# Kernel tuning notes

Measured on AMD Instinct MI355X. Metric: run time of the kernel, lower is better.

Reference implementation:

```python
import jax, jax.numpy as jnp
import numpy as np

GAMMA = 1.0          # smoothing parameter (init default)
NORMALIZE = False    # init default
BIG = 1e10           # finite stand-in for +inf boundary (exp(-BIG/gamma) == 0, grad-safe)


def setup_inputs() -> dict:
    key = jax.random.key(0)
    k1, k2 = jax.random.split(key)
    B, T, D = 64, 1024, 8
    pred = jax.random.normal(k1, (B, T, D), dtype=jnp.float32)
    target = jax.random.normal(k2, (B, T, D), dtype=jnp.float32)
    return {"pred": pred, "target": target}


def _soft_dtw(dist, gamma):
    # dist: [B, T, T] pairwise squared distances. Returns R[:, -1, -1] of shape [B].
    B, T, _ = dist.shape
    inv_g = 1.0 / gamma

    def inner_step(r_left, inp):
        # r_left = R[i, j-1]; r0 = R[i-1, j-1]; r1 = R[i-1, j]; d = D[i-1, j-1]
        r0, r1, d = inp  # each [B]
        stack = jnp.stack([r0, r1, r_left], axis=-1)          # [B, 3]
        rmin = -gamma * jax.nn.logsumexp(-stack * inv_g, axis=-1)
        val = d + rmin
        return val, val

    def outer_step(prev_row, d_row):
        # prev_row: [B, T+1] = R[i-1, :]; d_row: [B, T] = D[i-1, :]
        xs = (prev_row[:, :-1].T, prev_row[:, 1:].T, d_row.T)  # each [T, B]
        r_init = jnp.full((B,), BIG, dist.dtype)               # R[i, 0] = inf
        _, vals = jax.lax.scan(inner_step, r_init, xs)         # vals: [T, B]
        new_row = jnp.concatenate(
            [jnp.full((B, 1), BIG, dist.dtype), vals.T], axis=1)  # [B, T+1]
        return new_row, None

    # R[0, 0] = 0, R[0, j>0] = inf
    row0 = jnp.concatenate(
        [jnp.zeros((B, 1), dist.dtype), jnp.full((B, T), BIG, dist.dtype)], axis=1)
    last_row, _ = jax.lax.scan(outer_step, row0, jnp.transpose(dist, (1, 0, 2)))
    return last_row[:, -1]  # R[:, T, T]


def reference(pred, target):
    B, T, D = pred.shape
    # [B, T, T] squared Euclidean distance between all time-step pairs
    dist = jnp.sum((pred[:, :, None, :] - target[:, None, :, :]) ** 2, axis=-1)
    loss = _soft_dtw(dist, GAMMA)  # [B]
    if NORMALIZE:
        loss = loss / T
    return jnp.mean(loss)
```

## Files before the change

kernel.cpp:

```cpp
#include <hip/hip_runtime.h>


typedef float v2f __attribute__((ext_vector_type(2)));

static constexpr int T      = 1024;
static constexpr int NB     = 64;
static constexpr int NTH    = 256;
static constexpr int NW     = 4;
static constexpr int CT     = 2;
static constexpr int NQ     = T / CT;
static constexpr int WSTEPS = NQ + 63;

#define BIGF 1e10f
#define L2EF 1.4426950408889634f
#define LN2F 0.6931471805599453f

__device__ __forceinline__ float fexp2(float x) { return __builtin_amdgcn_exp2f(x); }
__device__ __forceinline__ float flog2(float x) { return __builtin_amdgcn_logf(x); }

__device__ __forceinline__ float softmin2(float a, float b, float c) {
  float m = fminf(fminf(a, b), c);
  float M = fmaxf(fmaxf(a, b), c);
  float e = __builtin_amdgcn_fmed3f(a, b, c);
  float s = fexp2(m - e) + fexp2(m - M);
  return m - flog2(1.0f + s);
}

__device__ __forceinline__ v2f pkfma(v2f a, v2f b, v2f c) {
  v2f d;
  asm("v_pk_fma_f32 %0, %1, %2, %3" : "=v"(d) : "v"(a), "v"(b), "v"(c));
  return d;
}

__device__ __forceinline__ v2f lo2(const float4& c) { v2f r; r.x = c.x; r.y = c.y; return r; }
__device__ __forceinline__ v2f hi2(const float4& c) { v2f r; r.x = c.z; r.y = c.w; return r; }

__device__ __forceinline__ v2f dotpk(v2f seed, const v2f* pp, const float4* C) {
  v2f a = seed;
  a = pkfma(pp[0], lo2(C[0]), a);
  a = pkfma(pp[1], hi2(C[0]), a);
  a = pkfma(pp[2], lo2(C[1]), a);
  a = pkfma(pp[3], hi2(C[1]), a);
  a = pkfma(pp[4], lo2(C[2]), a);
  a = pkfma(pp[5], hi2(C[2]), a);
  a = pkfma(pp[6], lo2(C[3]), a);
  a = pkfma(pp[7], hi2(C[3]), a);
  return a;
}

#define STEP(SW, CUR, NXT)                                                   \
  {                                                                          \
    const int sw_ = (SW);                                                    \
    float2 cb = make_float2(BIGF, BIGF);                                     \
    if (w > 0 && sw_ < NQ) {                                                 \
      if ((sw_ & 3) == 0) {                                                  \
        const int need = ((sw_ + 3 < NQ) ? sw_ + 3 : NQ - 1) + 63;           \
        while (seen < need) {                                                 \
          seen = __hip_atomic_load(&prog_s[w - 1], __ATOMIC_ACQUIRE,         \
                                   __HIP_MEMORY_SCOPE_WORKGROUP);            \
          if (seen < need) __builtin_amdgcn_s_sleep(1);                      \
        }                                                                    \
      }                                                                      \
      cb = buf_s[(w - 1) * NQ + sw_];       \
    }                                                                        \
    float na0 = __shfl_up(vD0, 1, 64);                                       \
    float na1 = __shfl_up(vD1, 1, 64);                                       \
    float a0 = (lane == 0) ? cb.x : na0;                                     \
    float a1 = (lane == 0) ? cb.y : na1;                                     \
    const int q = sw_ - lane;                                                \
    {            \
      int qn = sw_ + 1 - lane;                                               \
      qn = qn < 0 ? 0 : (qn > NQ - 1 ? NQ - 1 : qn);                         \
      const float4* bp = &tgt4_s[qn * 5];                                    \
      NXT[0] = bp[0]; NXT[1] = bp[1]; NXT[2] = bp[2]; NXT[3] = bp[3];        \
      NXT[4] = bp[4];                                                        \
    }                                                                        \
    if (q >= 0 && q < NQ) {                                                  \
      const float tn0 = CUR[4].x, tn1 = CUR[4].y;                            \
      v2f sA; sA.x = pnA + tn0; sA.y = pnA + tn1;                            \
      v2f sB; sB.x = pnB + tn0; sB.y = pnB + tn1;                            \
      v2f sC; sC.x = pnC + tn0; sC.y = pnC + tn1;                            \
      v2f sD; sD.x = pnD + tn0; sD.y = pnD + tn1;                            \
      v2f accA = dotpk(sA, ppA, CUR);                                        \
      v2f accB = dotpk(sB, ppB, CUR);                                        \
      v2f accC = dotpk(sC, ppC, CUR);                                        \
      v2f accD = dotpk(sD, ppD, CUR);                                        \
      float vA0 = accA.x + softmin2(carry, a0, lA);                          \
      float vA1 = accA.y + softmin2(a0, a1, vA0);                            \
      float vB0 = accB.x + softmin2(lA, vA0, lB);                            \
      float vB1 = accB.y + softmin2(vA0, vA1, vB0);                          \
      float vC0 = accC.x + softmin2(lB, vB0, lC);                            \
      float vC1 = accC.y + softmin2(vB0, vB1, vC0);                          \
      vD0 = accD.x + softmin2(lC, vC0, lD);                                  \
      vD1 = accD.y + softmin2(vC0, vC1, vD0);                                \
      lA = vA1; lB = vB1; lC = vC1; lD = vD1; carry = a1;                    \
      if (lane == 63 && w < NW - 1)                                          \
        buf_s[w * NQ + q] = make_float2(vD0, vD1);                           \
      if (t == NTH - 1 && q == NQ - 1) ws[b] = vD1 * LN2F;                   \
    }                                                                        \
    if (lane == 63 && w < NW - 1 && ((sw_ & 3) == 3 || sw_ == WSTEPS - 1))   \
      __hip_atomic_store(&prog_s[w], sw_, __ATOMIC_RELEASE,                  \
                         __HIP_MEMORY_SCOPE_WORKGROUP);                      \
  }

__global__ __launch_bounds__(NTH) void sdtw_kernel(const float* __restrict__ pred,
                                                   const float* __restrict__ target,
                                                   float* __restrict__ ws) {
  __shared__ float4 tgt4_s[NQ * 5];
  __shared__ float2 buf_s[(NW - 1) * NQ];
  __shared__ int prog_s[NW];

  const int t    = threadIdx.x;
  const int w    = t >> 6;
  const int lane = t & 63;
  const int b    = blockIdx.x;
  const float* pr = pred + (size_t)b * T * 8;
  const float* tg = target + (size_t)b * T * 8;

  {
    const float4* tg4 = reinterpret_cast<const float4*>(tg);
    const float s = -2.0f * L2EF;
#pragma unroll
    for (int h = 0; h < 2; ++h) {
      float4 u0 = tg4[t * 8 + 4 * h + 0];
      float4 u1 = tg4[t * 8 + 4 * h + 1];
      float4 u2 = tg4[t * 8 + 4 * h + 2];
      float4 u3 = tg4[t * 8 + 4 * h + 3];
      float tA = (u0.x * u0.x + u0.y * u0.y) + (u0.z * u0.z + u0.w * u0.w) +
                 (u1.x * u1.x + u1.y * u1.y) + (u1.z * u1.z + u1.w * u1.w);
      float tB = (u2.x * u2.x + u2.y * u2.y) + (u2.z * u2.z + u2.w * u2.w) +
                 (u3.x * u3.x + u3.y * u3.y) + (u3.z * u3.z + u3.w * u3.w);
      float4* dst = &tgt4_s[(2 * t + h) * 5];
      dst[0] = make_float4(u0.x * s, u2.x * s, u0.y * s, u2.y * s);
      dst[1] = make_float4(u0.z * s, u2.z * s, u0.w * s, u2.w * s);
      dst[2] = make_float4(u1.x * s, u3.x * s, u1.y * s, u3.y * s);
      dst[3] = make_float4(u1.z * s, u3.z * s, u1.w * s, u3.w * s);
      dst[4] = make_float4(tA * L2EF, tB * L2EF, 0.0f, 0.0f);
    }
  }
  if (t < NW) prog_s[t] = -1;

  const float4* pr4 = reinterpret_cast<const float4*>(pr);
  float4 qA0 = pr4[t * 8 + 0], qA1 = pr4[t * 8 + 1];
  float4 qB0 = pr4[t * 8 + 2], qB1 = pr4[t * 8 + 3];
  float4 qC0 = pr4[t * 8 + 4], qC1 = pr4[t * 8 + 5];
  float4 qD0 = pr4[t * 8 + 6], qD1 = pr4[t * 8 + 7];
#define NRM(a, b)                                                            \
  (((a.x * a.x + a.y * a.y) + (a.z * a.z + a.w * a.w) +                      \
    (b.x * b.x + b.y * b.y) + (b.z * b.z + b.w * b.w)) * L2EF)
  float pnA = NRM(qA0, qA1), pnB = NRM(qB0, qB1);
  float pnC = NRM(qC0, qC1), pnD = NRM(qD0, qD1);
#define DUP(pp, r0, r1)                                                      \
  pp[0].x = r0.x; pp[0].y = r0.x; pp[1].x = r0.y; pp[1].y = r0.y;            \
  pp[2].x = r0.z; pp[2].y = r0.z; pp[3].x = r0.w; pp[3].y = r0.w;            \
  pp[4].x = r1.x; pp[4].y = r1.x; pp[5].x = r1.y; pp[5].y = r1.y;            \
  pp[6].x = r1.z; pp[6].y = r1.z; pp[7].x = r1.w; pp[7].y = r1.w;
  v2f ppA[8], ppB[8], ppC[8], ppD[8];
  DUP(ppA, qA0, qA1) DUP(ppB, qB0, qB1) DUP(ppC, qC0, qC1) DUP(ppD, qD0, qD1)

  __syncthreads();

  float lA = BIGF, lB = BIGF, lC = BIGF, lD = BIGF;
  float carry = (t == 0) ? 0.0f : BIGF;
  float vD0 = BIGF, vD1 = BIGF;
  int seen = -1;

  float4 tgA[5], tgB[5];
  {
    tgA[0] = tgt4_s[0]; tgA[1] = tgt4_s[1]; tgA[2] = tgt4_s[2];
    tgA[3] = tgt4_s[3]; tgA[4] = tgt4_s[4];
  }

  for (int sw = 0; sw < 576; sw += 2) {
    STEP(sw, tgA, tgB)
    STEP(sw + 1, tgB, tgA)
  }
}

__global__ void sdtw_reduce(const float* __restrict__ ws, float* __restrict__ out) {
  int l = threadIdx.x;
  float v = ws[l];
#pragma unroll
  for (int k = 32; k >= 1; k >>= 1) v += __shfl_down(v, k, 64);
  if (l == 0) out[0] = v * (1.0f / (float)NB);
}

extern "C" void kernel_launch(void* const* d_in, const int* in_sizes, int n_in,
                              void* d_out, int out_size, void* d_ws, size_t ws_size,
                              hipStream_t stream) {
  const float* pred   = (const float*)d_in[0];
  const float* target = (const float*)d_in[1];
  float* out = (float*)d_out;
  float* ws  = (float*)d_ws;

  sdtw_kernel<<<NB, NTH, 0, stream>>>(pred, target, ws);
  sdtw_reduce<<<1, 64, 0, stream>>>(ws, out);
}
```

Before: 404.0 us.

## Process four target columns per lane per wavefront step and pipeline distance computation

Each lane now covers a 4x4 cell tile per step instead of 4x2, which cuts the wavefront step count from 576 to 320. The distance dot products for the next step are computed one step ahead into double-buffered registers, so they overlap with the serial softmin chain. Packed FMAs now use op_sel to broadcast pred elements instead of storing duplicated pairs. Sync between waves happens every 8 steps. The trade-off is more registers per thread (launch bounds set to 1) and a longer serial softmin chain per step.

```diff
diff --git a/kernel.cpp b/kernel.cpp
--- a/kernel.cpp
+++ b/kernel.cpp
@@ -7,7 +7,7 @@
 static constexpr int NB     = 64;
 static constexpr int NTH    = 256;
 static constexpr int NW     = 4;
-static constexpr int CT     = 2;
+static constexpr int CT     = 4;
 static constexpr int NQ     = T / CT;
 static constexpr int WSTEPS = NQ + 63;
 
@@ -26,88 +26,111 @@
   return m - flog2(1.0f + s);
 }
 
-__device__ __forceinline__ v2f pkfma(v2f a, v2f b, v2f c) {
+__device__ __forceinline__ v2f pkfma_lo(v2f a, v2f b, v2f c) {
   v2f d;
-  asm("v_pk_fma_f32 %0, %1, %2, %3" : "=v"(d) : "v"(a), "v"(b), "v"(c));
+  asm("v_pk_fma_f32 %0, %1, %2, %3 op_sel:[0,0,0] op_sel_hi:[0,1,1]"
+      : "=v"(d) : "v"(a), "v"(b), "v"(c));
+  return d;
+}
+__device__ __forceinline__ v2f pkfma_hi(v2f a, v2f b, v2f c) {
+  v2f d;
+  asm("v_pk_fma_f32 %0, %1, %2, %3 op_sel:[1,0,0] op_sel_hi:[1,1,1]"
+      : "=v"(d) : "v"(a), "v"(b), "v"(c));
   return d;
 }
 
 __device__ __forceinline__ v2f lo2(const float4& c) { v2f r; r.x = c.x; r.y = c.y; return r; }
 __device__ __forceinline__ v2f hi2(const float4& c) { v2f r; r.x = c.z; r.y = c.w; return r; }
 
-__device__ __forceinline__ v2f dotpk(v2f seed, const v2f* pp, const float4* C) {
-  v2f a = seed;
-  a = pkfma(pp[0], lo2(C[0]), a);
-  a = pkfma(pp[1], hi2(C[0]), a);
-  a = pkfma(pp[2], lo2(C[1]), a);
-  a = pkfma(pp[3], hi2(C[1]), a);
-  a = pkfma(pp[4], lo2(C[2]), a);
-  a = pkfma(pp[5], hi2(C[2]), a);
-  a = pkfma(pp[6], lo2(C[3]), a);
-  a = pkfma(pp[7], hi2(C[3]), a);
-  return a;
-}
-
-#define STEP(SW, CUR, NXT)                                                   \
+template <bool HI>
+__device__ __forceinline__ v2f dot8h(v2f acc, const v2f* Pp, const float4* TN) {
+#define CH(m) (HI ? hi2(TN[m]) : lo2(TN[m]))
+  acc = pkfma_lo(Pp[0], CH(0), acc);
+  acc = pkfma_hi(Pp[0], CH(1), acc);
+  acc = pkfma_lo(Pp[1], CH(2), acc);
+  acc = pkfma_hi(Pp[1], CH(3), acc);
+  acc = pkfma_lo(Pp[2], CH(4), acc);
+  acc = pkfma_hi(Pp[2], CH(5), acc);
+  acc = pkfma_lo(Pp[3], CH(6), acc);
+  acc = pkfma_hi(Pp[3], CH(7), acc);
+#undef CH
+  return acc;
+}
+
+#define STEP(SW, TC, TN, DC, DN)                                             \
   {                                                                          \
     const int sw_ = (SW);                                                    \
-    float2 cb = make_float2(BIGF, BIGF);                                     \
-    if (w > 0 && sw_ < NQ) {                                                 \
-      if ((sw_ & 3) == 0) {                                                  \
-        const int need = ((sw_ + 3 < NQ) ? sw_ + 3 : NQ - 1) + 63;           \
-        while (seen < need) {                                                 \
-          seen = __hip_atomic_load(&prog_s[w - 1], __ATOMIC_ACQUIRE,         \
-                                   __HIP_MEMORY_SCOPE_WORKGROUP);            \
-          if (seen < need) __builtin_amdgcn_s_sleep(1);                      \
-        }                                                                    \
+    if (w > 0 && sw_ < NQ && (sw_ & 7) == 0) {                               \
+      const int need = ((sw_ + 7 < NQ) ? sw_ + 7 : NQ - 1) + 63;             \
+      while (seen < need) {                                                   \
+        seen = __hip_atomic_load(&prog_s[w - 1], __ATOMIC_ACQUIRE,           \
+                                 __HIP_MEMORY_SCOPE_WORKGROUP);              \
+        if (seen < need) __builtin_amdgcn_s_sleep(1);                        \
       }                                                                      \
-      cb = buf_s[(w - 1) * NQ + sw_];       \
-    }                                                                        \
+    }                                                                        \
+    float4 cb = make_float4(BIGF, BIGF, BIGF, BIGF);                         \
+    if (w > 0 && sw_ < NQ) cb = buf_s[(w - 1) * NQ + sw_];                   \
     float na0 = __shfl_up(vD0, 1, 64);                                       \
     float na1 = __shfl_up(vD1, 1, 64);                                       \
-    float a0 = (lane == 0) ? cb.x : na0;                                     \
-    float a1 = (lane == 0) ? cb.y : na1;                                     \
+    float na2 = __shfl_up(vD2, 1, 64);                                       \
+    float na3 = __shfl_up(vD3, 1, 64);                                       \
+    const float a0 = (lane == 0) ? cb.x : na0;                               \
+    const float a1 = (lane == 0) ? cb.y : na1;                               \
+    const float a2 = (lane == 0) ? cb.z : na2;                               \
+    const float a3 = (lane == 0) ? cb.w : na3;                               \
     const int q = sw_ - lane;                                                \
-    {            \
-      int qn = sw_ + 1 - lane;                                               \
+    {                   \
+      int qn = sw_ + 2 - lane;                                               \
       qn = qn < 0 ? 0 : (qn > NQ - 1 ? NQ - 1 : qn);                         \
-      const float4* bp = &tgt4_s[qn * 5];                                    \
-      NXT[0] = bp[0]; NXT[1] = bp[1]; NXT[2] = bp[2]; NXT[3] = bp[3];        \
-      NXT[4] = bp[4];                                                        \
+      const float4* bp = &tgt4_s[qn * 9];                                    \
+      TC[0] = bp[0]; TC[1] = bp[1]; TC[2] = bp[2]; TC[3] = bp[3];            \
+      TC[4] = bp[4]; TC[5] = bp[5]; TC[6] = bp[6]; TC[7] = bp[7];            \
+      TC[8] = bp[8];                                                         \
+    }                                                                        \
+    {       \
+      const float4 nr = TN[8];                                               \
+      v2f s_;                                                                \
+      s_.x = pnA + nr.x; s_.y = pnA + nr.y; DN[0] = dot8h<false>(s_, ppA, TN); \
+      s_.x = pnA + nr.z; s_.y = pnA + nr.w; DN[1] = dot8h<true>(s_, ppA, TN);  \
+      s_.x = pnB + nr.x; s_.y = pnB + nr.y; DN[2] = dot8h<false>(s_, ppB, TN); \
+      s_.x = pnB + nr.z; s_.y = pnB + nr.w; DN[3] = dot8h<true>(s_, ppB, TN);  \
+      s_.x = pnC + nr.x; s_.y = pnC + nr.y; DN[4] = dot8h<false>(s_, ppC, TN); \
+      s_.x = pnC + nr.z; s_.y = pnC + nr.w; DN[5] = dot8h<true>(s_, ppC, TN);  \
+      s_.x = pnD + nr.x; s_.y = pnD + nr.y; DN[6] = dot8h<false>(s_, ppD, TN); \
+      s_.x = pnD + nr.z; s_.y = pnD + nr.w; DN[7] = dot8h<true>(s_, ppD, TN);  \
     }                                                                        \
     if (q >= 0 && q < NQ) {                                                  \
-      const float tn0 = CUR[4].x, tn1 = CUR[4].y;                            \
-      v2f sA; sA.x = pnA + tn0; sA.y = pnA + tn1;                            \
-      v2f sB; sB.x = pnB + tn0; sB.y = pnB + tn1;                            \
-      v2f sC; sC.x = pnC + tn0; sC.y = pnC + tn1;                            \
-      v2f sD; sD.x = pnD + tn0; sD.y = pnD + tn1;                            \
-      v2f accA = dotpk(sA, ppA, CUR);                                        \
-      v2f accB = dotpk(sB, ppB, CUR);                                        \
-      v2f accC = dotpk(sC, ppC, CUR);                                        \
-      v2f accD = dotpk(sD, ppD, CUR);                                        \
-      float vA0 = accA.x + softmin2(carry, a0, lA);                          \
-      float vA1 = accA.y + softmin2(a0, a1, vA0);                            \
-      float vB0 = accB.x + softmin2(lA, vA0, lB);                            \
-      float vB1 = accB.y + softmin2(vA0, vA1, vB0);                          \
-      float vC0 = accC.x + softmin2(lB, vB0, lC);                            \
-      float vC1 = accC.y + softmin2(vB0, vB1, vC0);                          \
-      vD0 = accD.x + softmin2(lC, vC0, lD);                                  \
-      vD1 = accD.y + softmin2(vC0, vC1, vD0);                                \
-      lA = vA1; lB = vB1; lC = vC1; lD = vD1; carry = a1;                    \
+      float vA0 = DC[0].x + softmin2(carry, a0, lA);                         \
+      float vA1 = DC[0].y + softmin2(a0, a1, vA0);                           \
+      float vA2 = DC[1].x + softmin2(a1, a2, vA1);                           \
+      float vA3 = DC[1].y + softmin2(a2, a3, vA2);                           \
+      float vB0 = DC[2].x + softmin2(lA, vA0, lB);                           \
+      float vB1 = DC[2].y + softmin2(vA0, vA1, vB0);                         \
+      float vB2 = DC[3].x + softmin2(vA1, vA2, vB1);                         \
+      float vB3 = DC[3].y + softmin2(vA2, vA3, vB2);                         \
+      float vC0 = DC[4].x + softmin2(lB, vB0, lC);                           \
+      float vC1 = DC[4].y + softmin2(vB0, vB1, vC0);                         \
+      float vC2 = DC[5].x + softmin2(vB1, vB2, vC1);                         \
+      float vC3 = DC[5].y + softmin2(vB2, vB3, vC2);                         \
+      vD0 = DC[6].x + softmin2(lC, vC0, lD);                                 \
+      vD1 = DC[6].y + softmin2(vC0, vC1, vD0);                               \
+      vD2 = DC[7].x + softmin2(vC1, vC2, vD1);                               \
+      vD3 = DC[7].y + softmin2(vC2, vC3, vD2);                               \
+      lA = vA3; lB = vB3; lC = vC3; lD = vD3; carry = a3;                    \
       if (lane == 63 && w < NW - 1)                                          \
-        buf_s[w * NQ + q] = make_float2(vD0, vD1);                           \
-      if (t == NTH - 1 && q == NQ - 1) ws[b] = vD1 * LN2F;                   \
-    }                                                                        \
-    if (lane == 63 && w < NW - 1 && ((sw_ & 3) == 3 || sw_ == WSTEPS - 1))   \
+        buf_s[w * NQ + q] = make_float4(vD0, vD1, vD2, vD3);                 \
+      if (t == NTH - 1 && q == NQ - 1) ws[b] = vD3 * LN2F;                   \
+    }                                                                        \
+    if (lane == 63 && w < NW - 1 && ((sw_ & 7) == 7 || sw_ == WSTEPS - 1))   \
       __hip_atomic_store(&prog_s[w], sw_, __ATOMIC_RELEASE,                  \
                          __HIP_MEMORY_SCOPE_WORKGROUP);                      \
   }
 
-__global__ __launch_bounds__(NTH) void sdtw_kernel(const float* __restrict__ pred,
-                                                   const float* __restrict__ target,
-                                                   float* __restrict__ ws) {
-  __shared__ float4 tgt4_s[NQ * 5];
-  __shared__ float2 buf_s[(NW - 1) * NQ];
+__global__ __launch_bounds__(NTH, 1) void sdtw_kernel(const float* __restrict__ pred,
+                                                      const float* __restrict__ target,
+                                                      float* __restrict__ ws) {
+  __shared__ float4 tgt4_s[NQ * 9];
+  __shared__ float4 buf_s[(NW - 1) * NQ];
   __shared__ int prog_s[NW];
 
   const int t    = threadIdx.x;
@@ -119,24 +142,26 @@
 
   {
     const float4* tg4 = reinterpret_cast<const float4*>(tg);
+    float4 u00 = tg4[t * 8 + 0], u01 = tg4[t * 8 + 1];
+    float4 u10 = tg4[t * 8 + 2], u11 = tg4[t * 8 + 3];
+    float4 u20 = tg4[t * 8 + 4], u21 = tg4[t * 8 + 5];
+    float4 u30 = tg4[t * 8 + 6], u31 = tg4[t * 8 + 7];
+#define NRM1(a, bq)                                                          \
+  (((a.x * a.x + a.y * a.y) + (a.z * a.z + a.w * a.w) +                      \
+    (bq.x * bq.x + bq.y * bq.y) + (bq.z * bq.z + bq.w * bq.w)))
+    float n0 = NRM1(u00, u01), n1 = NRM1(u10, u11);
+    float n2 = NRM1(u20, u21), n3 = NRM1(u30, u31);
     const float s = -2.0f * L2EF;
-#pragma unroll
-    for (int h = 0; h < 2; ++h) {
-      float4 u0 = tg4[t * 8 + 4 * h + 0];
-      float4 u1 = tg4[t * 8 + 4 * h + 1];
-      float4 u2 = tg4[t * 8 + 4 * h + 2];
-      float4 u3 = tg4[t * 8 + 4 * h + 3];
-      float tA = (u0.x * u0.x + u0.y * u0.y) + (u0.z * u0.z + u0.w * u0.w) +
-                 (u1.x * u1.x + u1.y * u1.y) + (u1.z * u1.z + u1.w * u1.w);
-      float tB = (u2.x * u2.x + u2.y * u2.y) + (u2.z * u2.z + u2.w * u2.w) +
-                 (u3.x * u3.x + u3.y * u3.y) + (u3.z * u3.z + u3.w * u3.w);
-      float4* dst = &tgt4_s[(2 * t + h) * 5];
-      dst[0] = make_float4(u0.x * s, u2.x * s, u0.y * s, u2.y * s);
-      dst[1] = make_float4(u0.z * s, u2.z * s, u0.w * s, u2.w * s);
-      dst[2] = make_float4(u1.x * s, u3.x * s, u1.y * s, u3.y * s);
-      dst[3] = make_float4(u1.z * s, u3.z * s, u1.w * s, u3.w * s);
-      dst[4] = make_float4(tA * L2EF, tB * L2EF, 0.0f, 0.0f);
-    }
+    float4* dst = &tgt4_s[t * 9];
+    dst[0] = make_float4(u00.x * s, u10.x * s, u20.x * s, u30.x * s);
+    dst[1] = make_float4(u00.y * s, u10.y * s, u20.y * s, u30.y * s);
+    dst[2] = make_float4(u00.z * s, u10.z * s, u20.z * s, u30.z * s);
+    dst[3] = make_float4(u00.w * s, u10.w * s, u20.w * s, u30.w * s);
+    dst[4] = make_float4(u01.x * s, u11.x * s, u21.x * s, u31.x * s);
+    dst[5] = make_float4(u01.y * s, u11.y * s, u21.y * s, u31.y * s);
+    dst[6] = make_float4(u01.z * s, u11.z * s, u21.z * s, u31.z * s);
+    dst[7] = make_float4(u01.w * s, u11.w * s, u21.w * s, u31.w * s);
+    dst[8] = make_float4(n0 * L2EF, n1 * L2EF, n2 * L2EF, n3 * L2EF);
   }
   if (t < NW) prog_s[t] = -1;
 
@@ -145,35 +170,46 @@
   float4 qB0 = pr4[t * 8 + 2], qB1 = pr4[t * 8 + 3];
   float4 qC0 = pr4[t * 8 + 4], qC1 = pr4[t * 8 + 5];
   float4 qD0 = pr4[t * 8 + 6], qD1 = pr4[t * 8 + 7];
-#define NRM(a, b)                                                            \
-  (((a.x * a.x + a.y * a.y) + (a.z * a.z + a.w * a.w) +                      \
-    (b.x * b.x + b.y * b.y) + (b.z * b.z + b.w * b.w)) * L2EF)
-  float pnA = NRM(qA0, qA1), pnB = NRM(qB0, qB1);
-  float pnC = NRM(qC0, qC1), pnD = NRM(qD0, qD1);
-#define DUP(pp, r0, r1)                                                      \
-  pp[0].x = r0.x; pp[0].y = r0.x; pp[1].x = r0.y; pp[1].y = r0.y;            \
-  pp[2].x = r0.z; pp[2].y = r0.z; pp[3].x = r0.w; pp[3].y = r0.w;            \
-  pp[4].x = r1.x; pp[4].y = r1.x; pp[5].x = r1.y; pp[5].y = r1.y;            \
-  pp[6].x = r1.z; pp[6].y = r1.z; pp[7].x = r1.w; pp[7].y = r1.w;
-  v2f ppA[8], ppB[8], ppC[8], ppD[8];
-  DUP(ppA, qA0, qA1) DUP(ppB, qB0, qB1) DUP(ppC, qC0, qC1) DUP(ppD, qD0, qD1)
+  float pnA = NRM1(qA0, qA1) * L2EF, pnB = NRM1(qB0, qB1) * L2EF;
+  float pnC = NRM1(qC0, qC1) * L2EF, pnD = NRM1(qD0, qD1) * L2EF;
+#define PAIRS(pp, r0, r1)                                                    \
+  pp[0] = lo2(r0); pp[1] = hi2(r0); pp[2] = lo2(r1); pp[3] = hi2(r1);
+  v2f ppA[4], ppB[4], ppC[4], ppD[4];
+  PAIRS(ppA, qA0, qA1) PAIRS(ppB, qB0, qB1)
+  PAIRS(ppC, qC0, qC1) PAIRS(ppD, qD0, qD1)
 
   __syncthreads();
 
   float lA = BIGF, lB = BIGF, lC = BIGF, lD = BIGF;
   float carry = (t == 0) ? 0.0f : BIGF;
-  float vD0 = BIGF, vD1 = BIGF;
+  float vD0 = BIGF, vD1 = BIGF, vD2 = BIGF, vD3 = BIGF;
   int seen = -1;
 
-  float4 tgA[5], tgB[5];
+  float4 tA[9], tB[9];
+  v2f dA[8], dB[8];
   {
-    tgA[0] = tgt4_s[0]; tgA[1] = tgt4_s[1]; tgA[2] = tgt4_s[2];
-    tgA[3] = tgt4_s[3]; tgA[4] = tgt4_s[4];
-  }
-
-  for (int sw = 0; sw < 576; sw += 2) {
-    STEP(sw, tgA, tgB)
-    STEP(sw + 1, tgB, tgA)
+    const float4* bp = &tgt4_s[0];
+    tA[0] = bp[0]; tA[1] = bp[1]; tA[2] = bp[2]; tA[3] = bp[3];
+    tA[4] = bp[4]; tA[5] = bp[5]; tA[6] = bp[6]; tA[7] = bp[7]; tA[8] = bp[8];
+    int q1 = 1 - lane; q1 = q1 < 0 ? 0 : q1;
+    const float4* bq = &tgt4_s[q1 * 9];
+    tB[0] = bq[0]; tB[1] = bq[1]; tB[2] = bq[2]; tB[3] = bq[3];
+    tB[4] = bq[4]; tB[5] = bq[5]; tB[6] = bq[6]; tB[7] = bq[7]; tB[8] = bq[8];
+    const float4 nr = tA[8];
+    v2f s_;
+    s_.x = pnA + nr.x; s_.y = pnA + nr.y; dA[0] = dot8h<false>(s_, ppA, tA);
+    s_.x = pnA + nr.z; s_.y = pnA + nr.w; dA[1] = dot8h<true>(s_, ppA, tA);
+    s_.x = pnB + nr.x; s_.y = pnB + nr.y; dA[2] = dot8h<false>(s_, ppB, tA);
+    s_.x = pnB + nr.z; s_.y = pnB + nr.w; dA[3] = dot8h<true>(s_, ppB, tA);
+    s_.x = pnC + nr.x; s_.y = pnC + nr.y; dA[4] = dot8h<false>(s_, ppC, tA);
+    s_.x = pnC + nr.z; s_.y = pnC + nr.w; dA[5] = dot8h<true>(s_, ppC, tA);
+    s_.x = pnD + nr.x; s_.y = pnD + nr.y; dA[6] = dot8h<false>(s_, ppD, tA);
+    s_.x = pnD + nr.z; s_.y = pnD + nr.w; dA[7] = dot8h<true>(s_, ppD, tA);
+  }
+
+  for (int sw = 0; sw < 320; sw += 2) {
+    STEP(sw, tA, tB, dA, dB)
+    STEP(sw + 1, tB, tA, dB, dA)
   }
 }
 
```

Result: slower. 474.7 us (+17.5%).
